# Kernel tuning notes

Hardware: AMD Instinct MI355X
Metric: run time of the kernel (lower is better)

## Reference

```python
import jax, jax.numpy as jnp
import numpy as np

BN_EPS = 1e-5


def cond_conv(x, att_w, att_b, weight, pad):
    """CondConv: per-sample expert-mixed conv.
    x: [N,C,H,W]; att_w: [K,C]; att_b: [K]; weight: [K,O,I,kh,kw]; pad: (ph,pw)."""
    pooled = x.mean(axis=(2, 3))                         # [N,C]  (AdaptiveAvgPool2d(1))
    att = jax.nn.sigmoid(pooled @ att_w.T + att_b)       # [N,K]  (1x1 conv + sigmoid)
    agg_w = jnp.einsum('nk,koihw->noihw', att, weight)   # per-sample kernels [N,O,I,kh,kw]

    def conv1(xi, wi):
        return jax.lax.conv_general_dilated(
            xi[None], wi, window_strides=(1, 1),
            padding=[(pad[0], pad[0]), (pad[1], pad[1])],
            dimension_numbers=('NCHW', 'OIHW', 'NCHW'))[0]

    return jax.vmap(conv1)(x, agg_w)                     # [N,O,H,W]


def batchnorm(x, gamma, beta):
    # training-mode BN: biased batch stats over (N,H,W)
    mean = x.mean(axis=(0, 2, 3), keepdims=True)
    var = x.var(axis=(0, 2, 3), keepdims=True)
    xn = (x - mean) * jax.lax.rsqrt(var + BN_EPS)
    return xn * gamma[None, :, None, None] + beta[None, :, None, None]


def channel_shuffle(x, g):
    N, C, H, W = x.shape
    return x.reshape(N, g, C // g, H, W).transpose(0, 2, 1, 3, 4).reshape(N, C, H, W)


def setup_inputs() -> dict:
    key = jax.random.key(0)
    ks = jax.random.split(key, 8)
    N, C, H, W = 32, 256, 64, 64
    Cb, K = C // 4, 4
    inp = {
        'x': jax.random.normal(ks[0], (N, C, H, W), jnp.float32),
        'sq_att_w': jax.random.normal(ks[1], (K, Cb), jnp.float32) * 0.1,
        'sq_att_b': jnp.zeros((K,), jnp.float32),
        'sq_w': jax.random.normal(ks[2], (K, Cb, Cb, 3, 3), jnp.float32) * 0.05,
        'sq_g': jnp.ones((Cb,), jnp.float32),
        'sq_b': jnp.zeros((Cb,), jnp.float32),
        'ver_att_w': jax.random.normal(ks[3], (K, Cb), jnp.float32) * 0.1,
        'ver_att_b': jnp.zeros((K,), jnp.float32),
        'ver_w': jax.random.normal(ks[4], (K, Cb, Cb, 3, 1), jnp.float32) * 0.05,
        'ver_g': jnp.ones((Cb,), jnp.float32),
        'ver_b': jnp.zeros((Cb,), jnp.float32),
        'hor_att_w': jax.random.normal(ks[5], (K, Cb), jnp.float32) * 0.1,
        'hor_att_b': jnp.zeros((K,), jnp.float32),
        'hor_w': jax.random.normal(ks[6], (K, Cb, Cb, 1, 3), jnp.float32) * 0.05,
        'hor_g': jnp.ones((Cb,), jnp.float32),
        'hor_b': jnp.zeros((Cb,), jnp.float32),
    }
    return inp


def reference(x, sq_att_w, sq_att_b, sq_w, sq_g, sq_b,
              ver_att_w, ver_att_b, ver_w, ver_g, ver_b,
              hor_att_w, hor_att_b, hor_w, hor_g, hor_b):
    # q_Split: chunk into 4 along channels
    s0, s1, s2, s3 = jnp.split(x, 4, axis=1)
    # square branch: CondConv 3x3 pad 1 + BN
    sq = batchnorm(cond_conv(s1, sq_att_w, sq_att_b, sq_w, (1, 1)), sq_g, sq_b)
    # vertical branch: CondConv 3x1 pad (1,0) + BN (crop layer is Identity since offset=0)
    ve = batchnorm(cond_conv(s2, ver_att_w, ver_att_b, ver_w, (1, 0)), ver_g, ver_b)
    # horizontal branch: CondConv 1x3 pad (0,1) + BN
    ho = batchnorm(cond_conv(s3, hor_att_w, hor_att_b, hor_w, (0, 1)), hor_g, hor_b)
    out = jnp.concatenate((s0, sq, ve, ho), axis=1)
    return channel_shuffle(out, 8)
```

## Files before the change

### kernel.cpp

```cpp
#include <hip/hip_runtime.h>
#include <cstddef>
#include <cstdint>


typedef __attribute__((ext_vector_type(8))) short frag8;
typedef __attribute__((ext_vector_type(16))) float accf16;

#define HW 4096
#define CNT_INV (1.0f / 131072.0f)

#define WS_POOLED 0
#define WS_ATT    6144
#define WS_SS     6528
#define WS_PST    6912
#define WS_WBF_SQ  203520
#define WS_WBF_VER 793344
#define WS_WBF_HOR 989952

__device__ __forceinline__ int shuf_ch(int c) { return ((c & 31) << 3) | (c >> 5); }

__device__ __forceinline__ unsigned bf16pair(float a, float b) {
    unsigned ua = __builtin_bit_cast(unsigned, a);
    unsigned ub = __builtin_bit_cast(unsigned, b);
    ua = (ua + 0x7fffu + ((ua >> 16) & 1u)) >> 16;
    ub = (ub + 0x7fffu + ((ub >> 16) & 1u)) >> 16;
    return ua | (ub << 16);
}

__global__ void __launch_bounds__(256) pool_kernel(const float* __restrict__ x,
                                                   float* __restrict__ pooled) {
    int bid = blockIdx.x;
    int c = bid & 63;
    int n = (bid >> 6) & 31;
    int b = bid >> 11;
    const float4* xp = (const float4*)(x + (size_t)(n * 256 + 64 * (b + 1) + c) * HW);
    int tid = threadIdx.x;
    float s = 0.f;
#pragma unroll
    for (int it = 0; it < 4; ++it) {
        float4 v = xp[tid + it * 256];
        s += (v.x + v.y) + (v.z + v.w);
    }
#pragma unroll
    for (int off = 32; off; off >>= 1) s += __shfl_down(s, off, 64);
    __shared__ float r[4];
    if ((tid & 63) == 0) r[tid >> 6] = s;
    __syncthreads();
    if (tid == 0) pooled[bid] = (r[0] + r[1] + r[2] + r[3]) * (1.f / 4096.f);
}

__global__ void __launch_bounds__(64) att_all_kernel(
    const float* __restrict__ pooled,
    const float* __restrict__ aw0, const float* __restrict__ ab0,
    const float* __restrict__ aw1, const float* __restrict__ ab1,
    const float* __restrict__ aw2, const float* __restrict__ ab2,
    float* __restrict__ att) {
    int bid = blockIdx.x;
    int b = bid >> 5;
    const float* aw = (b == 0) ? aw0 : (b == 1) ? aw1 : aw2;
    const float* ab = (b == 0) ? ab0 : (b == 1) ? ab1 : ab2;
    int t = threadIdx.x;
    float p = pooled[bid * 64 + t];
#pragma unroll
    for (int k = 0; k < 4; ++k) {
        float v = p * aw[k * 64 + t];
#pragma unroll
        for (int off = 32; off; off >>= 1) v += __shfl_down(v, off, 64);
        if (t == 0) att[bid * 4 + k] = 1.f / (1.f + expf(-(v + ab[k])));
    }
}

template <int TAPS>
__device__ __forceinline__ void aggbf_body(const float* __restrict__ w,
                                           const float* __restrict__ att,
                                           unsigned* __restrict__ wbf, int bid) {
    int idx = bid * 256 + threadIdx.x;
    int ip = idx & 31;
    int o  = (idx >> 5) & 63;
    int t  = (idx >> 11) % TAPS;
    int n  = (idx >> 11) / TAPS;
    const float* a = att + n * 4;
    constexpr int PS = 64 * 64 * TAPS;
    int base = (o * 64 + ip * 2) * TAPS + t;
    float v0 = a[0]*w[base] + a[1]*w[PS+base] + a[2]*w[2*PS+base] + a[3]*w[3*PS+base];
    int base1 = base + TAPS;
    float v1 = a[0]*w[base1] + a[1]*w[PS+base1] + a[2]*w[2*PS+base1] + a[3]*w[3*PS+base1];
    wbf[idx] = bf16pair(v0, v1);
}

__global__ void __launch_bounds__(256) aggbf_all_kernel(
    const float* __restrict__ sq_w, const float* __restrict__ ver_w,
    const float* __restrict__ hor_w, const float* __restrict__ att,
    unsigned* __restrict__ wsq, unsigned* __restrict__ wver,
    unsigned* __restrict__ whor) {
    int bid = blockIdx.x;
    if (bid < 2304)      aggbf_body<9>(sq_w,  att,       wsq,  bid);
    else if (bid < 3072) aggbf_body<3>(ver_w, att + 128, wver, bid - 2304);
    else                 aggbf_body<3>(hor_w, att + 256, whor, bid - 3072);
}

#define CSTR 1056
#define RSTR 8448

template <int KH, int KW, int PH, int PW>
__device__ __forceinline__ void conv_body(
    const float* __restrict__ x, const unsigned* __restrict__ wbf,
    float* __restrict__ out, float* __restrict__ pst, int cbase, int bid,
    unsigned char* xs, float (*red1)[2][2][16], float (*red2)[2][2][16]) {
    constexpr int TAPS = KH * KW;
    constexpr int HB = 4;
    constexpr int ROWS = HB + KH - 1;
    const int hb = bid & 15, n = bid >> 4;
    const int h0 = hb * HB;
    const int tid = threadIdx.x;
    const int lane = tid & 63;
    const int wv = tid >> 6;
    const int rh = wv >> 1, wn = wv & 1;
    const int l31 = lane & 31, hi = lane >> 5;
    const int wcol = wn * 32 + l31;

    if (KW > 1 && tid < ROWS * 16) {
        int r = tid >> 4, c = (tid >> 1) & 7, e = tid & 1;
        *(uint4*)(xs + r * RSTR + c * CSTR + (e ? 65 : 0) * 16) = uint4{0, 0, 0, 0};
    }

    {
        const int w = tid & 63, cg = tid >> 6;
        const float* xb = x + (size_t)(n * 256 + cbase) * HW;
        for (int r = 0; r < ROWS; ++r) {
            const int hin = h0 - PH + r;
            const bool rok = (KH == 1) || ((unsigned)hin < 64u);
#pragma unroll
            for (int half = 0; half < 2; ++half) {
                const int c = cg + half * 4;
                float v[8];
#pragma unroll
                for (int j = 0; j < 8; ++j)
                    v[j] = rok ? xb[(size_t)(c * 8 + j) * HW + hin * 64 + w] : 0.f;
                unsigned pk[4];
#pragma unroll
                for (int j = 0; j < 4; ++j) pk[j] = bf16pair(v[2 * j], v[2 * j + 1]);
                *(uint4*)(xs + r * RSTR + c * CSTR + (w + 1) * 16) = *(uint4*)pk;
            }
        }
    }

    const frag8* wp = (const frag8*)wbf + ((size_t)n * TAPS * 64 + l31) * 8 + hi;

    __syncthreads();

    accf16 a00 = {}, a01 = {}, a10 = {}, a11 = {};
#pragma unroll
    for (int t = 0; t < TAPS; ++t) {
        const int r_ = t / KW, dw = t % KW - PW;
        frag8 af[8];
#pragma unroll
        for (int kk = 0; kk < 4; ++kk) {
            af[kk]     = wp[t * 512 + kk * 2];
            af[4 + kk] = wp[t * 512 + 256 + kk * 2];
        }
        const unsigned char* bp = xs + (rh * 2 + r_) * RSTR + hi * CSTR +
                                  (wcol + dw + 1) * 16;
#pragma unroll
        for (int kk = 0; kk < 4; ++kk) {
            frag8 b0 = *(const frag8*)(bp + kk * 2 * CSTR);
            frag8 b1 = *(const frag8*)(bp + kk * 2 * CSTR + RSTR);
            a00 = __builtin_amdgcn_mfma_f32_32x32x16_bf16(af[kk],     b0, a00, 0, 0, 0);
            a10 = __builtin_amdgcn_mfma_f32_32x32x16_bf16(af[4 + kk], b0, a10, 0, 0, 0);
            a01 = __builtin_amdgcn_mfma_f32_32x32x16_bf16(af[kk],     b1, a01, 0, 0, 0);
            a11 = __builtin_amdgcn_mfma_f32_32x32x16_bf16(af[4 + kk], b1, a11, 0, 0, 0);
        }
    }

    {
        float* ob = out + (size_t)n * 256 * HW + (h0 + rh * 2) * 64 + wcol;
#pragma unroll
        for (int rg = 0; rg < 16; ++rg) {
            const int o = (rg & 3) + 8 * (rg >> 2) + 4 * hi;
            float* p0 = ob + (size_t)shuf_ch(cbase + o) * HW;
            p0[0]  = a00[rg];
            p0[64] = a01[rg];
            float* p1 = ob + (size_t)shuf_ch(cbase + 32 + o) * HW;
            p1[0]  = a10[rg];
            p1[64] = a11[rg];
        }
    }

#pragma unroll
    for (int rg = 0; rg < 16; ++rg) {
        float u1 = a00[rg] + a01[rg];
        float u2 = a00[rg] * a00[rg] + a01[rg] * a01[rg];
        float w1 = a10[rg] + a11[rg];
        float w2 = a10[rg] * a10[rg] + a11[rg] * a11[rg];
#pragma unroll
        for (int off = 16; off; off >>= 1) {
            u1 += __shfl_down(u1, off, 32);
            u2 += __shfl_down(u2, off, 32);
            w1 += __shfl_down(w1, off, 32);
            w2 += __shfl_down(w2, off, 32);
        }
        if (l31 == 0) {
            red1[wv][0][hi][rg] = u1; red2[wv][0][hi][rg] = u2;
            red1[wv][1][hi][rg] = w1; red2[wv][1][hi][rg] = w2;
        }
    }
    __syncthreads();
    if (tid < 64) {
        const int rg = tid & 15, hi2 = (tid >> 4) & 1, wm2 = tid >> 5;
        float s1 = 0.f, s2 = 0.f;
#pragma unroll
        for (int v = 0; v < 4; ++v) {
            s1 += red1[v][wm2][hi2][rg];
            s2 += red2[v][wm2][hi2][rg];
        }
        const int o = wm2 * 32 + (rg & 3) + 8 * (rg >> 2) + 4 * hi2;
        const int slot = n * 16 + hb;
        pst[o * 1024 + slot] = s1;
        pst[o * 1024 + 512 + slot] = s2;
    }
}

__device__ __forceinline__ void s0_body(const float* __restrict__ x,
                                        float* __restrict__ out, int bid) {
    const int n = bid >> 4, c0 = (bid & 15) * 4, tid = threadIdx.x;
#pragma unroll
    for (int j = 0; j < 4; ++j) {
        const int c = c0 + j;
        const float4* s = (const float4*)(x + (size_t)(n * 256 + c) * HW);
        float4* d = (float4*)(out + (size_t)(n * 256 + shuf_ch(c)) * HW);
#pragma unroll
        for (int it = 0; it < 4; ++it) d[tid + it * 256] = s[tid + it * 256];
    }
}

__global__ void __launch_bounds__(256, 3) conv_all_kernel(
    const float* __restrict__ x, const unsigned* __restrict__ wsq,
    const unsigned* __restrict__ wver, const unsigned* __restrict__ whor,
    float* __restrict__ out, float* __restrict__ pst) {
    __shared__ __align__(16) unsigned char xs[6 * RSTR];
    __shared__ float red1[4][2][2][16], red2[4][2][2][16];
    int bid = blockIdx.x;
    if (bid < 512)
        conv_body<3, 3, 1, 1>(x, wsq, out, pst, 64, bid, xs, red1, red2);
    else if (bid < 1024)
        conv_body<3, 1, 1, 0>(x, wver, out, pst + 65536, 128, bid - 512, xs, red1, red2);
    else if (bid < 1536)
        conv_body<1, 3, 0, 1>(x, whor, out, pst + 131072, 192, bid - 1024, xs, red1, red2);
    else
        s0_body(x, out, bid - 1536);
}

__global__ void __launch_bounds__(256) bnstats_all_kernel(
    const float* __restrict__ pst,
    const float* __restrict__ g0, const float* __restrict__ b0,
    const float* __restrict__ g1, const float* __restrict__ b1,
    const float* __restrict__ g2, const float* __restrict__ b2,
    float* __restrict__ ss) {
    int br = blockIdx.x >> 6, o = blockIdx.x & 63, t = threadIdx.x;
    const float* gamma = (br == 0) ? g0 : (br == 1) ? g1 : g2;
    const float* beta  = (br == 0) ? b0 : (br == 1) ? b1 : b2;
    const float* p = pst + br * 65536 + o * 1024;
    float s1 = 0.f, s2 = 0.f;
    for (int i = t; i < 512; i += 256) {
        s1 += p[i];
        s2 += p[512 + i];
    }
#pragma unroll
    for (int off = 32; off; off >>= 1) {
        s1 += __shfl_down(s1, off, 64);
        s2 += __shfl_down(s2, off, 64);
    }
    __shared__ float r1[4], r2[4];
    if ((t & 63) == 0) { r1[t >> 6] = s1; r2[t >> 6] = s2; }
    __syncthreads();
    if (t == 0) {
        float S1 = r1[0] + r1[1] + r1[2] + r1[3];
        float S2 = r2[0] + r2[1] + r2[2] + r2[3];
        float mean = S1 * CNT_INV;
        float var = S2 * CNT_INV - mean * mean;
        float scale = rsqrtf(var + 1e-5f) * gamma[o];
        ss[br * 128 + o * 2 + 0] = scale;
        ss[br * 128 + o * 2 + 1] = beta[o] - mean * scale;
    }
}

__global__ void __launch_bounds__(256) bn_all_kernel(float* __restrict__ out,
                                                     const float* __restrict__ ss) {
    int gbid = blockIdx.x;
    int sub = gbid >> 13;
    int bid = gbid & 8191;
    int chunk = bid & 3;
    int n = (bid >> 2) & 31;
    int o = bid >> 7;
    float scale = ss[sub * 128 + o * 2], shift = ss[sub * 128 + o * 2 + 1];
    int c_out = shuf_ch(64 * (sub + 1) + o);
    float4* p = (float4*)(out + (size_t)(n * 256 + c_out) * HW) + chunk * 256 + threadIdx.x;
    float4 v = *p;
    v.x = fmaf(v.x, scale, shift);
    v.y = fmaf(v.y, scale, shift);
    v.z = fmaf(v.z, scale, shift);
    v.w = fmaf(v.w, scale, shift);
    *p = v;
}

extern "C" void kernel_launch(void* const* d_in, const int* in_sizes, int n_in,
                              void* d_out, int out_size, void* d_ws, size_t ws_size,
                              hipStream_t stream) {
    const float* x        = (const float*)d_in[0];
    const float* sq_att_w = (const float*)d_in[1];
    const float* sq_att_b = (const float*)d_in[2];
    const float* sq_w     = (const float*)d_in[3];
    const float* sq_g     = (const float*)d_in[4];
    const float* sq_b     = (const float*)d_in[5];
    const float* ver_att_w= (const float*)d_in[6];
    const float* ver_att_b= (const float*)d_in[7];
    const float* ver_w    = (const float*)d_in[8];
    const float* ver_g    = (const float*)d_in[9];
    const float* ver_b    = (const float*)d_in[10];
    const float* hor_att_w= (const float*)d_in[11];
    const float* hor_att_b= (const float*)d_in[12];
    const float* hor_w    = (const float*)d_in[13];
    const float* hor_g    = (const float*)d_in[14];
    const float* hor_b    = (const float*)d_in[15];
    float* out = (float*)d_out;
    float* ws = (float*)d_ws;

    float* pooled = ws + WS_POOLED;
    float* att    = ws + WS_ATT;
    float* ss     = ws + WS_SS;
    float* pst    = ws + WS_PST;
    unsigned* wbf_sq  = (unsigned*)(ws + WS_WBF_SQ);
    unsigned* wbf_ver = (unsigned*)(ws + WS_WBF_VER);
    unsigned* wbf_hor = (unsigned*)(ws + WS_WBF_HOR);

    pool_kernel<<<6144, 256, 0, stream>>>(x, pooled);
    att_all_kernel<<<96, 64, 0, stream>>>(pooled, sq_att_w, sq_att_b,
                                          ver_att_w, ver_att_b,
                                          hor_att_w, hor_att_b, att);
    aggbf_all_kernel<<<3840, 256, 0, stream>>>(sq_w, ver_w, hor_w, att,
                                               wbf_sq, wbf_ver, wbf_hor);
    conv_all_kernel<<<2048, 256, 0, stream>>>(x, wbf_sq, wbf_ver, wbf_hor, out, pst);
    bnstats_all_kernel<<<192, 256, 0, stream>>>(pst, sq_g, sq_b, ver_g, ver_b,
                                                hor_g, hor_b, ss);
    bn_all_kernel<<<24576, 256, 0, stream>>>(out, ss);
}
```

Measured before the change: 154.5 us.

## Pre-convert branch inputs to padded bf16 LDS layout during pooling pass

```diff
diff --git a/kernel.cpp b/kernel.cpp
--- a/kernel.cpp
+++ b/kernel.cpp
@@ -8,6 +8,9 @@
 
 #define HW 4096
 #define CNT_INV (1.0f / 131072.0f)
+#define CSTR 1056
+#define RSTR 8448
+#define XT_BR (32ull * 66 * 8448)
 
 #define WS_POOLED 0
 #define WS_ATT    6144
@@ -16,6 +19,7 @@
 #define WS_WBF_SQ  203520
 #define WS_WBF_VER 793344
 #define WS_WBF_HOR 989952
+#define WS_XT      1186560
 
 __device__ __forceinline__ int shuf_ch(int c) { return ((c & 31) << 3) | (c >> 5); }
 
@@ -27,26 +31,56 @@
     return ua | (ub << 16);
 }
 
-__global__ void __launch_bounds__(256) pool_kernel(const float* __restrict__ x,
-                                                   float* __restrict__ pooled) {
-    int bid = blockIdx.x;
-    int c = bid & 63;
-    int n = (bid >> 6) & 31;
-    int b = bid >> 11;
-    const float4* xp = (const float4*)(x + (size_t)(n * 256 + 64 * (b + 1) + c) * HW);
-    int tid = threadIdx.x;
-    float s = 0.f;
-#pragma unroll
-    for (int it = 0; it < 4; ++it) {
-        float4 v = xp[tid + it * 256];
-        s += (v.x + v.y) + (v.z + v.w);
-    }
-#pragma unroll
-    for (int off = 32; off; off >>= 1) s += __shfl_down(s, off, 64);
-    __shared__ float r[4];
-    if ((tid & 63) == 0) r[tid >> 6] = s;
+__device__ __forceinline__ void gload_lds16(const void* g, void* l) {
+    __builtin_amdgcn_global_load_lds(
+        (const __attribute__((address_space(1))) void*)g,
+        (__attribute__((address_space(3))) void*)l, 16, 0, 0);
+}
+
+__global__ void __launch_bounds__(256) prepass_kernel(
+    const float* __restrict__ x, unsigned char* __restrict__ xt,
+    float* __restrict__ pooled) {
+    const int bid = blockIdx.x;
+    const int c8 = bid & 7;
+    const int n = (bid >> 3) & 31;
+    const int b = bid >> 8;
+    const int tid = threadIdx.x;
+    const int w = tid & 63, q = tid >> 6;
+    const float* xb = x + (size_t)(n * 256 + 64 * (b + 1) + c8 * 8) * HW;
+    unsigned char* xtb = xt + (size_t)b * XT_BR + (size_t)n * 66 * RSTR + c8 * CSTR;
+
+    float ps[8] = {0.f, 0.f, 0.f, 0.f, 0.f, 0.f, 0.f, 0.f};
+    for (int h = q; h < 64; h += 4) {
+        float v[8];
+#pragma unroll
+        for (int j = 0; j < 8; ++j) v[j] = xb[(size_t)j * HW + h * 64 + w];
+        unsigned pk[4];
+#pragma unroll
+        for (int j = 0; j < 4; ++j) pk[j] = bf16pair(v[2 * j], v[2 * j + 1]);
+        *(uint4*)(xtb + (size_t)(h + 1) * RSTR + (w + 1) * 16) = *(uint4*)pk;
+#pragma unroll
+        for (int j = 0; j < 8; ++j) ps[j] += v[j];
+    }
+    for (int idx = tid; idx < 260; idx += 256) {
+        int p, slot;
+        if (idx < 66)       { p = 0;         slot = idx; }
+        else if (idx < 132) { p = 65;        slot = idx - 66; }
+        else if (idx < 196) { p = idx - 131; slot = 0; }
+        else                { p = idx - 195; slot = 65; }
+        *(uint4*)(xtb + (size_t)p * RSTR + slot * 16) = uint4{0, 0, 0, 0};
+    }
+    __shared__ float red[4][8];
+#pragma unroll
+    for (int j = 0; j < 8; ++j)
+#pragma unroll
+        for (int off = 32; off; off >>= 1) ps[j] += __shfl_down(ps[j], off, 64);
+    if ((tid & 63) == 0)
+#pragma unroll
+        for (int j = 0; j < 8; ++j) red[q][j] = ps[j];
     __syncthreads();
-    if (tid == 0) pooled[bid] = (r[0] + r[1] + r[2] + r[3]) * (1.f / 4096.f);
+    if (tid < 8)
+        pooled[(b * 32 + n) * 64 + c8 * 8 + tid] =
+            (red[0][tid] + red[1][tid] + red[2][tid] + red[3][tid]) * (1.f / 4096.f);
 }
 
 __global__ void __launch_bounds__(64) att_all_kernel(
@@ -99,17 +133,16 @@
     else                 aggbf_body<3>(hor_w, att + 256, whor, bid - 3072);
 }
 
-#define CSTR 1056
-#define RSTR 8448
-
 template <int KH, int KW, int PH, int PW>
 __device__ __forceinline__ void conv_body(
-    const float* __restrict__ x, const unsigned* __restrict__ wbf,
+    const unsigned char* __restrict__ xt, const unsigned* __restrict__ wbf,
     float* __restrict__ out, float* __restrict__ pst, int cbase, int bid,
     unsigned char* xs, float (*red1)[2][2][16], float (*red2)[2][2][16]) {
     constexpr int TAPS = KH * KW;
     constexpr int HB = 4;
     constexpr int ROWS = HB + KH - 1;
+    constexpr int TOT = ROWS * RSTR;
+    constexpr int NCH = (TOT + 1023) >> 10;
     const int hb = bid & 15, n = bid >> 4;
     const int h0 = hb * HB;
     const int tid = threadIdx.x;
@@ -119,30 +152,12 @@
     const int l31 = lane & 31, hi = lane >> 5;
     const int wcol = wn * 32 + l31;
 
-    if (KW > 1 && tid < ROWS * 16) {
-        int r = tid >> 4, c = (tid >> 1) & 7, e = tid & 1;
-        *(uint4*)(xs + r * RSTR + c * CSTR + (e ? 65 : 0) * 16) = uint4{0, 0, 0, 0};
-    }
-
     {
-        const int w = tid & 63, cg = tid >> 6;
-        const float* xb = x + (size_t)(n * 256 + cbase) * HW;
-        for (int r = 0; r < ROWS; ++r) {
-            const int hin = h0 - PH + r;
-            const bool rok = (KH == 1) || ((unsigned)hin < 64u);
-#pragma unroll
-            for (int half = 0; half < 2; ++half) {
-                const int c = cg + half * 4;
-                float v[8];
-#pragma unroll
-                for (int j = 0; j < 8; ++j)
-                    v[j] = rok ? xb[(size_t)(c * 8 + j) * HW + hin * 64 + w] : 0.f;
-                unsigned pk[4];
-#pragma unroll
-                for (int j = 0; j < 4; ++j) pk[j] = bf16pair(v[2 * j], v[2 * j + 1]);
-                *(uint4*)(xs + r * RSTR + c * CSTR + (w + 1) * 16) = *(uint4*)pk;
-            }
-        }
+        const unsigned char* src = xt +
+            (size_t)(n * 66 + h0 + (KH == 1 ? 1 : 0)) * RSTR + lane * 16;
+#pragma unroll
+        for (int c = wv; c < NCH; c += 4)
+            gload_lds16(src + (c << 10), xs + (c << 10));
     }
 
     const frag8* wp = (const frag8*)wbf + ((size_t)n * TAPS * 64 + l31) * 8 + hi;
@@ -234,18 +249,21 @@
 }
 
 __global__ void __launch_bounds__(256, 3) conv_all_kernel(
-    const float* __restrict__ x, const unsigned* __restrict__ wsq,
-    const unsigned* __restrict__ wver, const unsigned* __restrict__ whor,
+    const float* __restrict__ x, const unsigned char* __restrict__ xt,
+    const unsigned* __restrict__ wsq, const unsigned* __restrict__ wver,
+    const unsigned* __restrict__ whor,
     float* __restrict__ out, float* __restrict__ pst) {
-    __shared__ __align__(16) unsigned char xs[6 * RSTR];
+    __shared__ __align__(16) unsigned char xs[6 * RSTR + 512];
     __shared__ float red1[4][2][2][16], red2[4][2][2][16];
     int bid = blockIdx.x;
     if (bid < 512)
-        conv_body<3, 3, 1, 1>(x, wsq, out, pst, 64, bid, xs, red1, red2);
+        conv_body<3, 3, 1, 1>(xt, wsq, out, pst, 64, bid, xs, red1, red2);
     else if (bid < 1024)
-        conv_body<3, 1, 1, 0>(x, wver, out, pst + 65536, 128, bid - 512, xs, red1, red2);
+        conv_body<3, 1, 1, 0>(xt + XT_BR, wver, out, pst + 65536, 128,
+                              bid - 512, xs, red1, red2);
     else if (bid < 1536)
-        conv_body<1, 3, 0, 1>(x, whor, out, pst + 131072, 192, bid - 1024, xs, red1, red2);
+        conv_body<1, 3, 0, 1>(xt + 2 * XT_BR, whor, out, pst + 131072, 192,
+                              bid - 1024, xs, red1, red2);
     else
         s0_body(x, out, bid - 1536);
 }
@@ -332,14 +350,16 @@
     unsigned* wbf_sq  = (unsigned*)(ws + WS_WBF_SQ);
     unsigned* wbf_ver = (unsigned*)(ws + WS_WBF_VER);
     unsigned* wbf_hor = (unsigned*)(ws + WS_WBF_HOR);
-
-    pool_kernel<<<6144, 256, 0, stream>>>(x, pooled);
+    unsigned char* xt = (unsigned char*)(ws + WS_XT);
+
+    prepass_kernel<<<768, 256, 0, stream>>>(x, xt, pooled);
     att_all_kernel<<<96, 64, 0, stream>>>(pooled, sq_att_w, sq_att_b,
                                           ver_att_w, ver_att_b,
                                           hor_att_w, hor_att_b, att);
     aggbf_all_kernel<<<3840, 256, 0, stream>>>(sq_w, ver_w, hor_w, att,
                                                wbf_sq, wbf_ver, wbf_hor);
-    conv_all_kernel<<<2048, 256, 0, stream>>>(x, wbf_sq, wbf_ver, wbf_hor, out, pst);
+    conv_all_kernel<<<2048, 256, 0, stream>>>(x, xt, wbf_sq, wbf_ver, wbf_hor,
+                                              out, pst);
     bnstats_all_kernel<<<192, 256, 0, stream>>>(pst, sq_g, sq_b, ver_g, ver_b,
                                                 hor_g, hor_b, ss);
     bn_all_kernel<<<24576, 256, 0, stream>>>(out, ss);
```

Result: slower. 163.2 us (+5.6%).
